# Kernel optimization log

Measured on AMD Instinct MI355X. Metric: run time of the kernel, lower is better.

Reference implementation:

```python
import jax, jax.numpy as jnp
import numpy as np

N_NODES = 500_000
N_EDGES = 16_000_000
D_COEF = 1  # init arg d
EPS = 1e-12  # F.normalize eps


def setup_inputs() -> dict:
    key = jax.random.key(0)
    k1, k2, k3 = jax.random.split(key, 3)
    theta = jax.random.normal(k1, (N_NODES, 1), dtype=jnp.float32)
    src = jax.random.randint(k2, (N_EDGES,), 0, N_NODES, dtype=jnp.int64)
    dst = jax.random.randint(k3, (N_EDGES,), 0, N_NODES, dtype=jnp.int64)
    v0 = jnp.ones((), dtype=jnp.float32)
    w0 = jnp.ones((), dtype=jnp.float32)
    return {"theta": theta, "src": src, "dst": dst, "v0": v0, "w0": w0}


def reference(theta, src, dst, v0, w0):
    # node velocity: v0 * [cos(theta), sin(theta)]  -> [N, 2]
    v = v0 * jnp.concatenate((jnp.cos(theta), jnp.sin(theta)), axis=-1)

    # edge message: dtheta = (theta_src - theta_dst) * d ; m = [cos, sin] -> [E, 2]
    dtheta = (theta[src, 0] - theta[dst, 0]) * D_COEF  # [E]
    m = jnp.stack((jnp.cos(dtheta), jnp.sin(dtheta)), axis=-1)  # [E, 2]

    # mailbox mean over incoming edges per destination node (segment mean)
    msum = jax.ops.segment_sum(m, dst, num_segments=N_NODES)  # [N, 2]
    cnt = jax.ops.segment_sum(jnp.ones((dst.shape[0],), m.dtype), dst,
                              num_segments=N_NODES)  # [N]
    mean_cs = msum / jnp.maximum(cnt, 1.0)[:, None]  # [N, 2]

    # torque: w0 * normalize(mean_cs, dim=-1)[..., 1:2]
    norm = jnp.linalg.norm(mean_cs, axis=-1, keepdims=True)
    unit = mean_cs / jnp.maximum(norm, EPS)
    torque = w0 * unit[:, 1:2]  # [N, 1]
    return v, torque
```

## Files before the change

### kernel.cpp

```cpp
#include <hip/hip_runtime.h>
#include <hip/hip_bf16.h>
#include <math.h>


#define NBITS_Q   21
#define Q_MASK    ((1u << NBITS_Q) - 1)
#define Q_SCALE   131072.0f
#define Q_INV     (1.0f / 131072.0f)
#define BIN_SHIFT 11
#define BIN_W     2048
#define NB        245
#define CAP       67584
#define K_BATCH   8192
#define EPT       32
#define SCALE_F   524288.0f
#define INV_SCALE (1.0f / 524288.0f)
#define INV_2PI   0.15915494309189535f

typedef unsigned uint4_v __attribute__((ext_vector_type(4)));

__global__ void init_cursors(unsigned* __restrict__ cur) {
    int b = blockIdx.x * blockDim.x + threadIdx.x;
    if (b < 256) cur[b] = (b < NB) ? (unsigned)b * CAP : 0u;
}

__global__ __launch_bounds__(256) void bin_edges_sort(
        const float* __restrict__ theta,
        const int4* __restrict__ src4, const int4* __restrict__ dst4,
        unsigned* __restrict__ bins, unsigned* __restrict__ cursor, int E)
{
    __shared__ unsigned      sorted[K_BATCH];
    __shared__ unsigned char sbin[K_BATCH];
    __shared__ unsigned      hist[256];
    __shared__ unsigned      base[256];
    __shared__ unsigned      gbase[256];

    const int tid   = threadIdx.x;
    const int bb    = blockIdx.x;
    const int e0    = bb * K_BATCH;
    const int nval  = min(K_BATCH, E - e0);
    const int E4    = E >> 2;
    const int base4 = e0 >> 2;

    hist[tid] = 0u;
    __syncthreads();

    int4 sQ[EPT / 4];
#pragma unroll
    for (int j = 0; j < EPT / 4; ++j) {
        const int idx4 = base4 + j * 256 + tid;
        sQ[j] = (idx4 < E4) ? src4[idx4] : make_int4(0, 0, 0, 0);
    }
    float tq[EPT];
#pragma unroll
    for (int j = 0; j < EPT / 4; ++j) {
        tq[j * 4 + 0] = theta[sQ[j].x];
        tq[j * 4 + 1] = theta[sQ[j].y];
        tq[j * 4 + 2] = theta[sQ[j].z];
        tq[j * 4 + 3] = theta[sQ[j].w];
    }

    unsigned ent[EPT];
    unsigned bnrk[EPT];
#pragma unroll
    for (int j = 0; j < EPT / 4; ++j) {
        const int idx4 = base4 + j * 256 + tid;
        const int q0   = j * 4;
        if (idx4 < E4) {
            const int4 d = dst4[idx4];
            const int dd[4] = {d.x, d.y, d.z, d.w};
#pragma unroll
            for (int k = 0; k < 4; ++k) {
                const unsigned b    = (unsigned)dd[k] >> BIN_SHIFT;
                const unsigned rank = atomicAdd(&hist[b], 1u);
                bnrk[q0 + k] = (b << 16) | rank;
                float qf = (tq[q0 + k] + 8.0f) * Q_SCALE + 0.5f;
                qf = fminf(fmaxf(qf, 0.0f), 2097151.0f);
                ent[q0 + k] = ((unsigned)(dd[k] & (BIN_W - 1)) << NBITS_Q)
                              | (unsigned)qf;
            }
        } else {
#pragma unroll
            for (int k = 0; k < 4; ++k) bnrk[q0 + k] = 0xFFFFFFFFu;
        }
    }
    __syncthreads();

    if (tid < 64) {
        unsigned h[4];
#pragma unroll
        for (int k = 0; k < 4; ++k) h[k] = hist[tid * 4 + k];
        const unsigned tot = h[0] + h[1] + h[2] + h[3];
        unsigned s = tot;
#pragma unroll
        for (int off = 1; off < 64; off <<= 1) {
            const unsigned y = __shfl_up(s, off);
            if (tid >= off) s += y;
        }
        unsigned run = s - tot;
#pragma unroll
        for (int k = 0; k < 4; ++k) {
            base[tid * 4 + k] = run;
            run += h[k];
        }
#pragma unroll
        for (int k = 0; k < 4; ++k)
            if (h[k]) gbase[tid * 4 + k] = atomicAdd(&cursor[tid * 4 + k], h[k]);
    }
    __syncthreads();

#pragma unroll
    for (int q = 0; q < EPT; ++q) {
        if (bnrk[q] != 0xFFFFFFFFu) {
            const unsigned b   = bnrk[q] >> 16;
            const unsigned pos = base[b] + (bnrk[q] & 0xFFFFu);
            sorted[pos] = ent[q];
            sbin[pos]   = (unsigned char)b;
        }
    }
    __syncthreads();

    for (int l = tid; l < nval; l += 256) {
        const unsigned b    = sbin[l];
        const unsigned gpos = gbase[b] + ((unsigned)l - base[b]);
        if (gpos < (b + 1u) * CAP)
            bins[gpos] = sorted[l];
    }
}

__global__ __launch_bounds__(1024) void reduce_bins(
        const float* __restrict__ theta, const unsigned* __restrict__ bins,
        const unsigned* __restrict__ cursor, const float* __restrict__ v0p,
        const float* __restrict__ w0p, float* __restrict__ out, int N)
{
    __shared__ float th[BIN_W];
    __shared__ unsigned long long acc[BIN_W];
    const int b     = blockIdx.x;
    const int tid   = threadIdx.x;
    const int node0 = b * BIN_W;
    const int W     = min(BIN_W, N - node0);

    for (int j = tid; j < BIN_W; j += 1024) {
        th[j]  = (j < W) ? theta[node0 + j] : 0.f;
        acc[j] = 0ull;
    }
    __syncthreads();

    const unsigned  base  = (unsigned)b * CAP;
    const int       count = (int)(cursor[b] - base);
    const unsigned* bp    = bins + base;

    const int CH = 1024 * 8;
    int i0 = 0;
    for (; i0 + CH <= count; i0 += CH) {
        const uint4_v ea = __builtin_nontemporal_load(
            (const uint4_v*)(bp + i0 + tid * 4));
        const uint4_v eb = __builtin_nontemporal_load(
            (const uint4_v*)(bp + i0 + 4096 + tid * 4));
        const unsigned ee[8] = {ea.x, ea.y, ea.z, ea.w, eb.x, eb.y, eb.z, eb.w};
#pragma unroll
        for (int k = 0; k < 8; ++k) {
            const unsigned e = ee[k];
            const unsigned l = e >> NBITS_Q;
            const float ts = (float)(e & Q_MASK) * Q_INV - 8.0f;
            const float r  = (ts - th[l]) * INV_2PI;
            const float sn = __builtin_amdgcn_sinf(r);
            const float cs = __builtin_amdgcn_cosf(r);
            const unsigned cq = (unsigned)((cs + 1.0f) * SCALE_F + 0.5f);
            const unsigned sq = (unsigned)((sn + 1.0f) * SCALE_F + 0.5f);
            atomicAdd(&acc[l], (1ull << 56) | ((unsigned long long)cq << 28)
                               | (unsigned long long)sq);
        }
    }
    for (int i = i0 + tid; i < count; i += 1024) {
        const unsigned e = __builtin_nontemporal_load(bp + i);
        const unsigned l = e >> NBITS_Q;
        const float ts = (float)(e & Q_MASK) * Q_INV - 8.0f;
        const float r  = (ts - th[l]) * INV_2PI;
        const float sn = __builtin_amdgcn_sinf(r);
        const float cs = __builtin_amdgcn_cosf(r);
        const unsigned cq = (unsigned)((cs + 1.0f) * SCALE_F + 0.5f);
        const unsigned sq = (unsigned)((sn + 1.0f) * SCALE_F + 0.5f);
        atomicAdd(&acc[l], (1ull << 56) | ((unsigned long long)cq << 28)
                           | (unsigned long long)sq);
    }
    __syncthreads();

    const float v0 = *v0p, w0 = *w0p;
    for (int j = tid; j < W; j += 1024) {
        const float t  = th[j];
        const float rr = t * INV_2PI;
        const float sn = __builtin_amdgcn_sinf(rr);
        const float cs = __builtin_amdgcn_cosf(rr);
        ((float2*)out)[node0 + j] = make_float2(v0 * cs, v0 * sn);
        const unsigned long long P = acc[j];
        const float c  = (float)(unsigned)(P >> 56);
        const float xs = (float)(unsigned)((P >> 28) & 0xFFFFFFFull) * INV_SCALE - c;
        const float ys = (float)(unsigned)(P & 0xFFFFFFFull) * INV_SCALE - c;
        const float nrm = sqrtf(xs * xs + ys * ys);
        out[2 * N + node0 + j] = w0 * (ys / fmaxf(nrm, 1e-12f));
    }
}


__global__ void zero_ws_kernel(float4* __restrict__ ws, int n4) {
    int i = blockIdx.x * blockDim.x + threadIdx.x;
    if (i < n4) ws[i] = make_float4(0.f, 0.f, 0.f, 0.f);
}

__global__ void edge_kernel_fb(const float* __restrict__ theta,
                               const int4* __restrict__ src4,
                               const int4* __restrict__ dst4,
                               float2* __restrict__ acc, int E8) {
    int i = blockIdx.x * blockDim.x + threadIdx.x;
    if (i >= E8) return;
    const int4 s0 = src4[2 * i], s1 = src4[2 * i + 1];
    const int4 d0 = dst4[2 * i], d1 = dst4[2 * i + 1];
    const int ss[8] = {s0.x, s0.y, s0.z, s0.w, s1.x, s1.y, s1.z, s1.w};
    const int dd[8] = {d0.x, d0.y, d0.z, d0.w, d1.x, d1.y, d1.z, d1.w};
    float ts[8], td[8];
#pragma unroll
    for (int k = 0; k < 8; ++k) ts[k] = theta[ss[k]];
#pragma unroll
    for (int k = 0; k < 8; ++k) td[k] = theta[dd[k]];
#pragma unroll
    for (int k = 0; k < 8; ++k) {
        float sn, cs;
        __sincosf(ts[k] - td[k], &sn, &cs);
        atomicAdd(&acc[dd[k]].x, cs);
        atomicAdd(&acc[dd[k]].y, sn);
    }
}

__global__ void node_kernel_fb(const float* __restrict__ theta,
                               const float2* __restrict__ acc,
                               const float* __restrict__ v0p,
                               const float* __restrict__ w0p,
                               float* __restrict__ out, int N) {
    int i = blockIdx.x * blockDim.x + threadIdx.x;
    if (i >= N) return;
    const float v0 = *v0p, w0 = *w0p;
    float sn, cs;
    __sincosf(theta[i], &sn, &cs);
    ((float2*)out)[i] = make_float2(v0 * cs, v0 * sn);
    const float2 a = acc[i];
    const float nrm = sqrtf(a.x * a.x + a.y * a.y);
    out[2 * N + i] = w0 * (a.y / fmaxf(nrm, 1e-12f));
}

extern "C" void kernel_launch(void* const* d_in, const int* in_sizes, int n_in,
                              void* d_out, int out_size, void* d_ws, size_t ws_size,
                              hipStream_t stream) {
    const float* theta = (const float*)d_in[0];
    const int*   src   = (const int*)d_in[1];
    const int*   dst   = (const int*)d_in[2];
    const float* v0p   = (const float*)d_in[3];
    const float* w0p   = (const float*)d_in[4];
    float*       out   = (float*)d_out;

    const int N = in_sizes[0];
    const int E = in_sizes[1];

    const size_t need = 1024 + (size_t)NB * CAP * sizeof(unsigned);

    if (ws_size >= need && N <= NB * BIN_W) {
        unsigned* cursor = (unsigned*)d_ws;
        unsigned* bins   = cursor + 256;

        init_cursors<<<1, 256, 0, stream>>>(cursor);

        const int nblk = (E + K_BATCH - 1) / K_BATCH;
        bin_edges_sort<<<nblk, 256, 0, stream>>>(theta, (const int4*)src,
                                                 (const int4*)dst,
                                                 bins, cursor, E);

        const int nbins = (N + BIN_W - 1) / BIN_W;
        reduce_bins<<<nbins, 1024, 0, stream>>>(theta, bins, cursor,
                                                v0p, w0p, out, N);
    } else {
        float2* acc = (float2*)d_ws;
        {
            const int n4 = (2 * N) / 4;
            zero_ws_kernel<<<(n4 + 255) / 256, 256, 0, stream>>>((float4*)d_ws, n4);
        }
        {
            const int E8 = E / 8;
            edge_kernel_fb<<<(E8 + 255) / 256, 256, 0, stream>>>(
                theta, (const int4*)src, (const int4*)dst, acc, E8);
        }
        node_kernel_fb<<<(N + 255) / 256, 256, 0, stream>>>(theta, acc, v0p, w0p,
                                                            out, N);
    }
}
```

Measured before the change: 327.3 us.

## Make edge binning persistent with software-pipelined prefetch of next chunk

The binning kernel becomes persistent with a fixed grid of 768 blocks. Each block walks chunks of 4096 edges and double-buffers register state, prefetching the next chunk's src/dst indices and theta gathers while it sorts and scatters the current chunk. Local ranks now come from a second shared atomic counter instead of the histogram atomic's return value. The aim is to hide gather latency, at the cost of more registers, extra barriers and a smaller batch per sort, which can make the global scatter less coalesced.

```diff
diff --git a/kernel.cpp b/kernel.cpp
--- a/kernel.cpp
+++ b/kernel.cpp
@@ -11,8 +11,9 @@
 #define BIN_W     2048
 #define NB        245
 #define CAP       67584
-#define K_BATCH   8192
-#define EPT       32
+#define K_BATCH   4096
+#define EPT       16
+#define NBLK_P1   768
 #define SCALE_F   524288.0f
 #define INV_SCALE (1.0f / 524288.0f)
 #define INV_2PI   0.15915494309189535f
@@ -32,99 +33,154 @@
     __shared__ unsigned      sorted[K_BATCH];
     __shared__ unsigned char sbin[K_BATCH];
     __shared__ unsigned      hist[256];
-    __shared__ unsigned      base[256];
+    __shared__ unsigned      base_[256];
     __shared__ unsigned      gbase[256];
-
-    const int tid   = threadIdx.x;
-    const int bb    = blockIdx.x;
-    const int e0    = bb * K_BATCH;
-    const int nval  = min(K_BATCH, E - e0);
-    const int E4    = E >> 2;
-    const int base4 = e0 >> 2;
+    __shared__ unsigned      lcnt[256];
+
+    const int tid    = threadIdx.x;
+    const int E4     = E >> 2;
+    const int NCHUNK = (E + K_BATCH - 1) / K_BATCH;
 
     hist[tid] = 0u;
+    lcnt[tid] = 0u;
+
+    int4  dQA[EPT / 4], dQZ[EPT / 4];
+    float tqA[EPT],     tqZ[EPT];
+
+    int c = blockIdx.x;
+    {
+        int4 sQ[EPT / 4];
+        const int cb4 = c * (K_BATCH >> 2);
+#pragma unroll
+        for (int j = 0; j < EPT / 4; ++j) {
+            const int idx4 = cb4 + j * 256 + tid;
+            if (idx4 < E4) { sQ[j] = src4[idx4]; dQA[j] = dst4[idx4]; }
+            else           { sQ[j] = make_int4(0,0,0,0); dQA[j] = make_int4(0,0,0,0); }
+        }
+#pragma unroll
+        for (int j = 0; j < EPT / 4; ++j) {
+            tqA[j * 4 + 0] = theta[sQ[j].x];
+            tqA[j * 4 + 1] = theta[sQ[j].y];
+            tqA[j * 4 + 2] = theta[sQ[j].z];
+            tqA[j * 4 + 3] = theta[sQ[j].w];
+        }
+    }
     __syncthreads();
 
-    int4 sQ[EPT / 4];
-#pragma unroll
-    for (int j = 0; j < EPT / 4; ++j) {
-        const int idx4 = base4 + j * 256 + tid;
-        sQ[j] = (idx4 < E4) ? src4[idx4] : make_int4(0, 0, 0, 0);
-    }
-    float tq[EPT];
-#pragma unroll
-    for (int j = 0; j < EPT / 4; ++j) {
-        tq[j * 4 + 0] = theta[sQ[j].x];
-        tq[j * 4 + 1] = theta[sQ[j].y];
-        tq[j * 4 + 2] = theta[sQ[j].z];
-        tq[j * 4 + 3] = theta[sQ[j].w];
-    }
-
-    unsigned ent[EPT];
-    unsigned bnrk[EPT];
-#pragma unroll
-    for (int j = 0; j < EPT / 4; ++j) {
-        const int idx4 = base4 + j * 256 + tid;
-        const int q0   = j * 4;
-        if (idx4 < E4) {
-            const int4 d = dst4[idx4];
-            const int dd[4] = {d.x, d.y, d.z, d.w};
-#pragma unroll
-            for (int k = 0; k < 4; ++k) {
-                const unsigned b    = (unsigned)dd[k] >> BIN_SHIFT;
-                const unsigned rank = atomicAdd(&hist[b], 1u);
-                bnrk[q0 + k] = (b << 16) | rank;
-                float qf = (tq[q0 + k] + 8.0f) * Q_SCALE + 0.5f;
-                qf = fminf(fmaxf(qf, 0.0f), 2097151.0f);
-                ent[q0 + k] = ((unsigned)(dd[k] & (BIN_W - 1)) << NBITS_Q)
-                              | (unsigned)qf;
-            }
-        } else {
-#pragma unroll
-            for (int k = 0; k < 4; ++k) bnrk[q0 + k] = 0xFFFFFFFFu;
-        }
-    }
-    __syncthreads();
-
-    if (tid < 64) {
-        unsigned h[4];
-#pragma unroll
-        for (int k = 0; k < 4; ++k) h[k] = hist[tid * 4 + k];
-        const unsigned tot = h[0] + h[1] + h[2] + h[3];
-        unsigned s = tot;
-#pragma unroll
-        for (int off = 1; off < 64; off <<= 1) {
-            const unsigned y = __shfl_up(s, off);
-            if (tid >= off) s += y;
-        }
-        unsigned run = s - tot;
-#pragma unroll
-        for (int k = 0; k < 4; ++k) {
-            base[tid * 4 + k] = run;
-            run += h[k];
-        }
-#pragma unroll
-        for (int k = 0; k < 4; ++k)
-            if (h[k]) gbase[tid * 4 + k] = atomicAdd(&cursor[tid * 4 + k], h[k]);
-    }
-    __syncthreads();
-
-#pragma unroll
-    for (int q = 0; q < EPT; ++q) {
-        if (bnrk[q] != 0xFFFFFFFFu) {
-            const unsigned b   = bnrk[q] >> 16;
-            const unsigned pos = base[b] + (bnrk[q] & 0xFFFFu);
-            sorted[pos] = ent[q];
-            sbin[pos]   = (unsigned char)b;
-        }
-    }
-    __syncthreads();
-
-    for (int l = tid; l < nval; l += 256) {
-        const unsigned b    = sbin[l];
-        const unsigned gpos = gbase[b] + ((unsigned)l - base[b]);
-        if (gpos < (b + 1u) * CAP)
-            bins[gpos] = sorted[l];
+    bool done = false;
+    while (!done) {
+#pragma unroll
+        for (int par = 0; par < 2; ++par) {
+            int4*  dQ  = (par == 0) ? dQA : dQZ;
+            float* tq  = (par == 0) ? tqA : tqZ;
+            int4*  dQn = (par == 0) ? dQZ : dQA;
+            float* tqn = (par == 0) ? tqZ : tqA;
+
+            if (done) continue;
+
+            const int cn = c + NBLK_P1;
+
+            int4 sQn[EPT / 4];
+            const bool have_next = (cn < NCHUNK);
+            if (have_next) {
+                const int nb4 = cn * (K_BATCH >> 2);
+#pragma unroll
+                for (int j = 0; j < EPT / 4; ++j) {
+                    const int idx4 = nb4 + j * 256 + tid;
+                    if (idx4 < E4) { sQn[j] = src4[idx4]; dQn[j] = dst4[idx4]; }
+                    else { sQn[j] = make_int4(0,0,0,0); dQn[j] = make_int4(0,0,0,0); }
+                }
+            }
+
+            const int cb4 = c * (K_BATCH >> 2);
+            unsigned ent[EPT];
+            unsigned bn[EPT];
+#pragma unroll
+            for (int j = 0; j < EPT / 4; ++j) {
+                const int idx4 = cb4 + j * 256 + tid;
+                const int q0   = j * 4;
+                if (idx4 < E4) {
+                    const int dd[4] = {dQ[j].x, dQ[j].y, dQ[j].z, dQ[j].w};
+#pragma unroll
+                    for (int k = 0; k < 4; ++k) {
+                        const unsigned b = (unsigned)dd[k] >> BIN_SHIFT;
+                        float qf = (tq[q0 + k] + 8.0f) * Q_SCALE + 0.5f;
+                        qf = fminf(fmaxf(qf, 0.0f), 2097151.0f);
+                        ent[q0 + k] = ((unsigned)(dd[k] & (BIN_W - 1)) << NBITS_Q)
+                                      | (unsigned)qf;
+                        bn[q0 + k]  = b;
+                        atomicAdd(&hist[b], 1u);
+                    }
+                } else {
+#pragma unroll
+                    for (int k = 0; k < 4; ++k) bn[q0 + k] = 0xFFu;
+                }
+            }
+            __syncthreads();
+
+            if (have_next) {
+#pragma unroll
+                for (int j = 0; j < EPT / 4; ++j) {
+                    tqn[j * 4 + 0] = theta[sQn[j].x];
+                    tqn[j * 4 + 1] = theta[sQn[j].y];
+                    tqn[j * 4 + 2] = theta[sQn[j].z];
+                    tqn[j * 4 + 3] = theta[sQn[j].w];
+                }
+            }
+
+            unsigned hC[4], gbC[4];
+            if (tid < 64) {
+#pragma unroll
+                for (int k = 0; k < 4; ++k) hC[k] = hist[tid * 4 + k];
+                const unsigned tot = hC[0] + hC[1] + hC[2] + hC[3];
+                unsigned s = tot;
+#pragma unroll
+                for (int off = 1; off < 64; off <<= 1) {
+                    const unsigned y = __shfl_up(s, off);
+                    if (tid >= off) s += y;
+                }
+                unsigned run = s - tot;
+#pragma unroll
+                for (int k = 0; k < 4; ++k) {
+                    base_[tid * 4 + k] = run;
+                    run += hC[k];
+                }
+#pragma unroll
+                for (int k = 0; k < 4; ++k)
+                    gbC[k] = hC[k] ? atomicAdd(&cursor[tid * 4 + k], hC[k]) : 0u;
+            }
+            __syncthreads();
+
+#pragma unroll
+            for (int q = 0; q < EPT; ++q) {
+                if (bn[q] != 0xFFu) {
+                    const unsigned b   = bn[q];
+                    const unsigned pos = base_[b] + atomicAdd(&lcnt[b], 1u);
+                    sorted[pos] = ent[q];
+                    sbin[pos]   = (unsigned char)b;
+                }
+            }
+            if (tid < 64) {
+#pragma unroll
+                for (int k = 0; k < 4; ++k)
+                    if (hC[k]) gbase[tid * 4 + k] = gbC[k];
+            }
+            __syncthreads();
+
+            const int nval = min(K_BATCH, E - c * K_BATCH);
+            for (int l = tid; l < nval; l += 256) {
+                const unsigned b    = sbin[l];
+                const unsigned gpos = gbase[b] + ((unsigned)l - base_[b]);
+                if (gpos < (b + 1u) * CAP)
+                    bins[gpos] = sorted[l];
+            }
+            hist[tid] = 0u;
+            lcnt[tid] = 0u;
+            __syncthreads();
+
+            c = cn;
+            if (!have_next) done = true;
+        }
     }
 }
 
@@ -269,10 +325,9 @@
 
         init_cursors<<<1, 256, 0, stream>>>(cursor);
 
-        const int nblk = (E + K_BATCH - 1) / K_BATCH;
-        bin_edges_sort<<<nblk, 256, 0, stream>>>(theta, (const int4*)src,
-                                                 (const int4*)dst,
-                                                 bins, cursor, E);
+        bin_edges_sort<<<NBLK_P1, 256, 0, stream>>>(theta, (const int4*)src,
+                                                    (const int4*)dst,
+                                                    bins, cursor, E);
 
         const int nbins = (N + BIN_W - 1) / BIN_W;
         reduce_bins<<<nbins, 1024, 0, stream>>>(theta, bins, cursor,
```

After: 453.1 us. 38.4% more time.

## Bin edges by source index and use a precomputed cos/sin table with angle-difference identity

Applied to the files above, without the earlier changes.

Adds a new default path. A small kernel first builds a per-node (cos, sin) table and writes the velocity output from it. The binning pass then stores the source index instead of a quantized theta, so it no longer gathers theta, and the in-bin rank comes from a second shared atomic pass instead of the first atomic's return value. The reduce pass gathers cos/sin of the source from the table and accumulates packed fixed-point sums. The destination rotation is applied once per node through the angle-difference identity, which removes per-edge transcendentals in exchange for an 8-byte random table gather per edge.

```diff
diff --git a/kernel.cpp b/kernel.cpp
--- a/kernel.cpp
+++ b/kernel.cpp
@@ -3,6 +3,8 @@
 #include <math.h>
 
 
+#define NBITS_S   19
+#define SRC_MASK  ((1u << NBITS_S) - 1)
 #define NBITS_Q   21
 #define Q_MASK    ((1u << NBITS_Q) - 1)
 #define Q_SCALE   131072.0f
@@ -24,7 +26,183 @@
     if (b < 256) cur[b] = (b < NB) ? (unsigned)b * CAP : 0u;
 }
 
-__global__ __launch_bounds__(256) void bin_edges_sort(
+__global__ __launch_bounds__(256) void build_table(
+        const float* __restrict__ theta, const float* __restrict__ v0p,
+        float2* __restrict__ table, float* __restrict__ out, int N)
+{
+    const int i = blockIdx.x * blockDim.x + threadIdx.x;
+    if (i >= N) return;
+    const float t = theta[i];
+    float sn, cs;
+    __sincosf(t, &sn, &cs);
+    table[i] = make_float2(cs, sn);
+    const float v0 = *v0p;
+    ((float2*)out)[i] = make_float2(v0 * cs, v0 * sn);
+}
+
+__global__ __launch_bounds__(256) void bin_edges_sort_src(
+        const int4* __restrict__ src4, const int4* __restrict__ dst4,
+        unsigned* __restrict__ bins, unsigned* __restrict__ cursor, int E)
+{
+    __shared__ unsigned      sorted[K_BATCH];
+    __shared__ unsigned char sbin[K_BATCH];
+    __shared__ unsigned      hist[256];
+    __shared__ unsigned      base[256];
+    __shared__ unsigned      gbase[256];
+    __shared__ unsigned      lcnt[256];
+
+    const int tid   = threadIdx.x;
+    const int bb    = blockIdx.x;
+    const int e0    = bb * K_BATCH;
+    const int nval  = min(K_BATCH, E - e0);
+    const int E4    = E >> 2;
+    const int base4 = e0 >> 2;
+
+    hist[tid] = 0u;
+    lcnt[tid] = 0u;
+    __syncthreads();
+
+    int4 sQ[EPT / 4], dQ[EPT / 4];
+#pragma unroll
+    for (int j = 0; j < EPT / 4; ++j) {
+        const int idx4 = base4 + j * 256 + tid;
+        if (idx4 < E4) { sQ[j] = src4[idx4]; dQ[j] = dst4[idx4]; }
+        else           { sQ[j] = make_int4(0,0,0,0); dQ[j] = make_int4(0,0,0,0); }
+    }
+
+    unsigned ent[EPT];
+    unsigned bn[EPT];
+#pragma unroll
+    for (int j = 0; j < EPT / 4; ++j) {
+        const int idx4 = base4 + j * 256 + tid;
+        const int q0   = j * 4;
+        if (idx4 < E4) {
+            const int dd[4] = {dQ[j].x, dQ[j].y, dQ[j].z, dQ[j].w};
+            const int ss[4] = {sQ[j].x, sQ[j].y, sQ[j].z, sQ[j].w};
+#pragma unroll
+            for (int k = 0; k < 4; ++k) {
+                const unsigned b = (unsigned)dd[k] >> BIN_SHIFT;
+                ent[q0 + k] = ((unsigned)(dd[k] & (BIN_W - 1)) << NBITS_S)
+                              | (unsigned)ss[k];
+                bn[q0 + k]  = b;
+                atomicAdd(&hist[b], 1u);
+            }
+        } else {
+#pragma unroll
+            for (int k = 0; k < 4; ++k) bn[q0 + k] = 0xFFu;
+        }
+    }
+    __syncthreads();
+
+    if (tid < 64) {
+        unsigned h[4];
+#pragma unroll
+        for (int k = 0; k < 4; ++k) h[k] = hist[tid * 4 + k];
+        const unsigned tot = h[0] + h[1] + h[2] + h[3];
+        unsigned s = tot;
+#pragma unroll
+        for (int off = 1; off < 64; off <<= 1) {
+            const unsigned y = __shfl_up(s, off);
+            if (tid >= off) s += y;
+        }
+        unsigned run = s - tot;
+#pragma unroll
+        for (int k = 0; k < 4; ++k) {
+            base[tid * 4 + k] = run;
+            run += h[k];
+        }
+#pragma unroll
+        for (int k = 0; k < 4; ++k)
+            if (h[k]) gbase[tid * 4 + k] = atomicAdd(&cursor[tid * 4 + k], h[k]);
+    }
+    __syncthreads();
+
+#pragma unroll
+    for (int q = 0; q < EPT; ++q) {
+        if (bn[q] != 0xFFu) {
+            const unsigned b   = bn[q];
+            const unsigned pos = base[b] + atomicAdd(&lcnt[b], 1u);
+            sorted[pos] = ent[q];
+            sbin[pos]   = (unsigned char)b;
+        }
+    }
+    __syncthreads();
+
+    for (int l = tid; l < nval; l += 256) {
+        const unsigned b    = sbin[l];
+        const unsigned gpos = gbase[b] + ((unsigned)l - base[b]);
+        if (gpos < (b + 1u) * CAP)
+            bins[gpos] = sorted[l];
+    }
+}
+
+__global__ __launch_bounds__(1024) void reduce_bins_tab(
+        const float2* __restrict__ table, const unsigned* __restrict__ bins,
+        const unsigned* __restrict__ cursor, const float* __restrict__ w0p,
+        float* __restrict__ out, int N)
+{
+    __shared__ unsigned long long acc[BIN_W];
+    const int b     = blockIdx.x;
+    const int tid   = threadIdx.x;
+    const int node0 = b * BIN_W;
+    const int W     = min(BIN_W, N - node0);
+
+    for (int j = tid; j < BIN_W; j += 1024) acc[j] = 0ull;
+    __syncthreads();
+
+    const unsigned  base  = (unsigned)b * CAP;
+    const int       count = (int)(cursor[b] - base);
+    const unsigned* bp    = bins + base;
+
+    const int CH = 1024 * 8;
+    int i0 = 0;
+    for (; i0 + CH <= count; i0 += CH) {
+        const uint4_v ea = __builtin_nontemporal_load(
+            (const uint4_v*)(bp + i0 + tid * 4));
+        const uint4_v eb = __builtin_nontemporal_load(
+            (const uint4_v*)(bp + i0 + 4096 + tid * 4));
+        const unsigned ee[8] = {ea.x, ea.y, ea.z, ea.w, eb.x, eb.y, eb.z, eb.w};
+        float2 ts[8];
+#pragma unroll
+        for (int k = 0; k < 8; ++k) ts[k] = table[ee[k] & SRC_MASK];
+#pragma unroll
+        for (int k = 0; k < 8; ++k) {
+            const unsigned l  = ee[k] >> NBITS_S;
+            const unsigned cq = (unsigned)__builtin_fmaf(ts[k].x, SCALE_F,
+                                                         SCALE_F + 0.5f);
+            const unsigned sq = (unsigned)__builtin_fmaf(ts[k].y, SCALE_F,
+                                                         SCALE_F + 0.5f);
+            atomicAdd(&acc[l], (1ull << 56) | ((unsigned long long)cq << 28)
+                               | (unsigned long long)sq);
+        }
+    }
+    for (int i = i0 + tid; i < count; i += 1024) {
+        const unsigned e  = __builtin_nontemporal_load(bp + i);
+        const unsigned l  = e >> NBITS_S;
+        const float2  tsv = table[e & SRC_MASK];
+        const unsigned cq = (unsigned)__builtin_fmaf(tsv.x, SCALE_F,
+                                                     SCALE_F + 0.5f);
+        const unsigned sq = (unsigned)__builtin_fmaf(tsv.y, SCALE_F,
+                                                     SCALE_F + 0.5f);
+        atomicAdd(&acc[l], (1ull << 56) | ((unsigned long long)cq << 28)
+                           | (unsigned long long)sq);
+    }
+    __syncthreads();
+
+    const float w0 = *w0p;
+    for (int j = tid; j < W; j += 1024) {
+        const unsigned long long P = acc[j];
+        const float c = (float)(unsigned)(P >> 56);
+        const float C = (float)(unsigned)((P >> 28) & 0xFFFFFFFull) * INV_SCALE - c;
+        const float S = (float)(unsigned)(P & 0xFFFFFFFull) * INV_SCALE - c;
+        const float2 td = table[node0 + j];
+        const float nrm = sqrtf(C * C + S * S);
+        out[2 * N + node0 + j] = w0 * ((td.x * S - td.y * C) / fmaxf(nrm, 1e-12f));
+    }
+}
+
+
+__global__ __launch_bounds__(256) void bin_edges_sort_thq(
         const float* __restrict__ theta,
         const int4* __restrict__ src4, const int4* __restrict__ dst4,
         unsigned* __restrict__ bins, unsigned* __restrict__ cursor, int E)
@@ -34,6 +212,7 @@
     __shared__ unsigned      hist[256];
     __shared__ unsigned      base[256];
     __shared__ unsigned      gbase[256];
+    __shared__ unsigned      lcnt[256];
 
     const int tid   = threadIdx.x;
     const int bb    = blockIdx.x;
@@ -43,6 +222,7 @@
     const int base4 = e0 >> 2;
 
     hist[tid] = 0u;
+    lcnt[tid] = 0u;
     __syncthreads();
 
     int4 sQ[EPT / 4];
@@ -61,7 +241,7 @@
     }
 
     unsigned ent[EPT];
-    unsigned bnrk[EPT];
+    unsigned bn[EPT];
 #pragma unroll
     for (int j = 0; j < EPT / 4; ++j) {
         const int idx4 = base4 + j * 256 + tid;
@@ -71,17 +251,17 @@
             const int dd[4] = {d.x, d.y, d.z, d.w};
 #pragma unroll
             for (int k = 0; k < 4; ++k) {
-                const unsigned b    = (unsigned)dd[k] >> BIN_SHIFT;
-                const unsigned rank = atomicAdd(&hist[b], 1u);
-                bnrk[q0 + k] = (b << 16) | rank;
+                const unsigned b = (unsigned)dd[k] >> BIN_SHIFT;
                 float qf = (tq[q0 + k] + 8.0f) * Q_SCALE + 0.5f;
                 qf = fminf(fmaxf(qf, 0.0f), 2097151.0f);
                 ent[q0 + k] = ((unsigned)(dd[k] & (BIN_W - 1)) << NBITS_Q)
                               | (unsigned)qf;
+                bn[q0 + k]  = b;
+                atomicAdd(&hist[b], 1u);
             }
         } else {
 #pragma unroll
-            for (int k = 0; k < 4; ++k) bnrk[q0 + k] = 0xFFFFFFFFu;
+            for (int k = 0; k < 4; ++k) bn[q0 + k] = 0xFFu;
         }
     }
     __syncthreads();
@@ -111,9 +291,9 @@
 
 #pragma unroll
     for (int q = 0; q < EPT; ++q) {
-        if (bnrk[q] != 0xFFFFFFFFu) {
-            const unsigned b   = bnrk[q] >> 16;
-            const unsigned pos = base[b] + (bnrk[q] & 0xFFFFu);
+        if (bn[q] != 0xFFu) {
+            const unsigned b   = bn[q];
+            const unsigned pos = base[b] + atomicAdd(&lcnt[b], 1u);
             sorted[pos] = ent[q];
             sbin[pos]   = (unsigned char)b;
         }
@@ -128,7 +308,7 @@
     }
 }
 
-__global__ __launch_bounds__(1024) void reduce_bins(
+__global__ __launch_bounds__(1024) void reduce_bins_thq(
         const float* __restrict__ theta, const unsigned* __restrict__ bins,
         const unsigned* __restrict__ cursor, const float* __restrict__ v0p,
         const float* __restrict__ w0p, float* __restrict__ out, int N)
@@ -261,22 +441,37 @@
     const int N = in_sizes[0];
     const int E = in_sizes[1];
 
-    const size_t need = 1024 + (size_t)NB * CAP * sizeof(unsigned);
-
-    if (ws_size >= need && N <= NB * BIN_W) {
+    const size_t bins_bytes = (size_t)NB * CAP * sizeof(unsigned);
+    const size_t tab_bytes  = (((size_t)N * 8) + 1023) & ~(size_t)1023;
+    const size_t need_thq   = 1024 + bins_bytes;
+    const size_t need_tab   = tab_bytes + 1024 + bins_bytes;
+
+    const int nblk  = (E + K_BATCH - 1) / K_BATCH;
+    const int nbins = (N + BIN_W - 1) / BIN_W;
+
+    if (ws_size >= need_tab && N <= NB * BIN_W && N <= (1 << NBITS_S)) {
+        float2*   table  = (float2*)d_ws;
+        unsigned* cursor = (unsigned*)((char*)d_ws + tab_bytes);
+        unsigned* bins   = cursor + 256;
+
+        init_cursors<<<1, 256, 0, stream>>>(cursor);
+        build_table<<<(N + 255) / 256, 256, 0, stream>>>(theta, v0p, table,
+                                                         out, N);
+        bin_edges_sort_src<<<nblk, 256, 0, stream>>>((const int4*)src,
+                                                     (const int4*)dst,
+                                                     bins, cursor, E);
+        reduce_bins_tab<<<nbins, 1024, 0, stream>>>(table, bins, cursor,
+                                                    w0p, out, N);
+    } else if (ws_size >= need_thq && N <= NB * BIN_W) {
         unsigned* cursor = (unsigned*)d_ws;
         unsigned* bins   = cursor + 256;
 
         init_cursors<<<1, 256, 0, stream>>>(cursor);
-
-        const int nblk = (E + K_BATCH - 1) / K_BATCH;
-        bin_edges_sort<<<nblk, 256, 0, stream>>>(theta, (const int4*)src,
-                                                 (const int4*)dst,
-                                                 bins, cursor, E);
-
-        const int nbins = (N + BIN_W - 1) / BIN_W;
-        reduce_bins<<<nbins, 1024, 0, stream>>>(theta, bins, cursor,
-                                                v0p, w0p, out, N);
+        bin_edges_sort_thq<<<nblk, 256, 0, stream>>>(theta, (const int4*)src,
+                                                     (const int4*)dst,
+                                                     bins, cursor, E);
+        reduce_bins_thq<<<nbins, 1024, 0, stream>>>(theta, bins, cursor,
+                                                    v0p, w0p, out, N);
     } else {
         float2* acc = (float2*)d_ws;
         {
```

After: 355.9 us. 8.7% more time.
